# Kernel tuning notes

Hardware: AMD Instinct MI355X
Metric: run time of the kernel (lower is better)

Reference implementation:

```python
import jax, jax.numpy as jnp
import numpy as np

KERNEL_SIZE = (5, 5)  # kernel_size repeated over dim=2 -> K = 25
DEGREE = 1            # linear B-spline
IS_OPEN = (1, 1)      # open splines in both pseudo-coordinate dims


def spline_basis(pseudo):
    """Degree-1 B-spline basis, matching torch_spline_conv SplineBasis.
    pseudo: [E, D] in [0, 1]. Returns basis [E, S], weight_index [E, S],
    with S = (degree+1)^D."""
    E, D = pseudo.shape
    m = DEGREE
    S = (m + 1) ** D
    ks = jnp.asarray(KERNEL_SIZE, dtype=jnp.int32)
    open_ = jnp.asarray(IS_OPEN, dtype=jnp.int32)
    v = pseudo * (ks - m * open_).astype(pseudo.dtype)          # [E, D]
    fl = jnp.floor(v)
    frac = v - fl                                                # fractional part
    fl = fl.astype(jnp.int32)
    # k_mod[s, d] = (s // (m+1)^d) % (m+1)  (mixed-radix digit)
    s_ids = jnp.arange(S, dtype=jnp.int32)
    radix = (m + 1) ** jnp.arange(D, dtype=jnp.int32)
    k_mod = (s_ids[:, None] // radix[None, :]) % (m + 1)         # [S, D]
    # degree-1 basis: k_mod==0 -> 1-frac ; k_mod==1 -> frac
    b = jnp.where(k_mod[None] == 0, 1.0 - frac[:, None, :], frac[:, None, :])  # [E,S,D]
    basis = jnp.prod(b, axis=-1)                                 # [E, S]
    # weight index: mixed-radix over kernel dims with wrap-around mod ks
    offs = jnp.concatenate([jnp.ones((1,), jnp.int32), jnp.cumprod(ks)[:-1]])  # [D]
    wi = jnp.sum(((fl[:, None, :] + k_mod[None]) % ks) * offs, axis=-1)        # [E, S]
    return basis, wi


def setup_inputs() -> dict:
    key = jax.random.key(0)
    k1, k2, k3, k4 = jax.random.split(key, 4)
    B, N, Fin, Fout, K = 8, 4096, 64, 64, 25
    x = jax.random.normal(k1, (B, N, Fin), dtype=jnp.float32)
    coord = jax.random.uniform(k2, (B, N, 2), dtype=jnp.float32)
    mask = jnp.ones((B, N), dtype=jnp.float32)
    weight = jax.random.normal(k3, (K, Fin, Fout), dtype=jnp.float32) * (1.0 / np.sqrt(K * Fin))
    root = jax.random.normal(k4, (Fin, Fout), dtype=jnp.float32) * (1.0 / np.sqrt(K * Fin))
    bias = jnp.zeros((Fout,), dtype=jnp.float32)
    return {"x": x, "coord": coord, "mask": mask, "weight": weight, "root": root, "bias": bias}


def reference(x, coord, mask, weight, root, bias):
    B, N, F = x.shape
    E = B * N
    x2 = x.reshape(E, F)
    basis, wi = spline_basis(coord.reshape(E, coord.shape[-1]))   # [E,S], [E,S]
    nan = jnp.isnan(basis)
    basis = jnp.where(nan, 0.0, basis)
    wi = jnp.where(nan, 0, wi)
    # SplineWeighting: out[e,o] = sum_s basis[e,s] * (x[e] @ weight[wi[e,s]])
    proj = jnp.einsum('ef,kfo->keo', x2, weight)                  # [K, E, O]
    gath = proj[wi, jnp.arange(E)[:, None], :]                    # [E, S, O]
    out = jnp.einsum('es,eso->eo', basis, gath)                   # [E, O]
    out = out + x2 @ root                                         # root (self) transform
    out = out.reshape(B, N, -1) + bias
    out = out * mask[..., None]                                   # 2D mask path
    return out
```

## Files before the change

### kernel.cpp

```cpp
#include <hip/hip_runtime.h>
#include <hip/hip_bf16.h>


#define NACT  16
#define NPREP 32
#define CAP_B 128
#define NTILE 40

typedef __attribute__((ext_vector_type(8))) short bhalf8;
typedef __attribute__((ext_vector_type(4))) float f32x4;

__device__ __forceinline__ unsigned short f2bf(float f) {
    return __builtin_bit_cast(unsigned short, __float2bfloat16(f));
}

__global__ __launch_bounds__(1024) void k_prep(
    const float* __restrict__ coord, const float* __restrict__ weight,
    const float* __restrict__ root,
    int* __restrict__ cnt2, int* __restrict__ idx2,
    unsigned short* __restrict__ wtab, int E)
{
    __shared__ int lcnt[NACT];
    int tid = threadIdx.x, blk = blockIdx.x;
    if (tid < NACT) lcnt[tid] = 0;
    __syncthreads();
    int e = blk * 1024 + tid;
    int c = 0, lpos = 0;
    if (e < E) {
        float2 cc = *(const float2*)(coord + 2 * e);
        int i0 = (int)floorf(cc.x * 4.0f); if (i0 > 3) i0 = 3; if (i0 < 0) i0 = 0;
        int i1 = (int)floorf(cc.y * 4.0f); if (i1 > 3) i1 = 3; if (i1 < 0) i1 = 0;
        c = i0 + 4 * i1;
        lpos = atomicAdd(&lcnt[c], 1);
    }
    __syncthreads();
    if (e < E && lpos < CAP_B) idx2[(c * NPREP + blk) * CAP_B + lpos] = e;
    if (tid < NACT) {
        int v = lcnt[tid];
        cnt2[tid * NPREP + blk] = v < CAP_B ? v : CAP_B;
    }

    if (tid < 400) {
        int gi = blk * 400 + tid;
        int k = gi >> 9;
        int r = gi & 511;
        int o = r >> 3, g = r & 7;
        const float* wsrc = weight + k * 4096;
        bhalf8 u8;
        #pragma unroll
        for (int j = 0; j < 8; ++j) {
            int f = g * 8 + j;
            u8[j] = f2bf(wsrc[f * 64 + o] + root[f * 64 + o]);
        }
        *(bhalf8*)((char*)wtab + k * 8192 + o * 128 + ((g ^ (o & 7)) << 4)) = u8;
    }
}

__global__ __launch_bounds__(256) void k_main(
    const float* __restrict__ x, const float* __restrict__ coord,
    const float* __restrict__ mask, const float* __restrict__ bias,
    const int* __restrict__ cnt2, const int* __restrict__ idx2,
    const unsigned short* __restrict__ wtab, float* __restrict__ out)
{
    __shared__ __align__(16) unsigned short xs[64 * 64];
    __shared__ __align__(16) unsigned short wt[4 * 64 * 64];
    __shared__ float4 bsv[64];
    __shared__ float  msk[64];
    __shared__ int    eid[64];
    __shared__ float  bsh[64];
    __shared__ int    sprefix[NPREP + 1];

    int tid = threadIdx.x;
    int lane = tid & 63, wv = tid >> 6;

    int u = blockIdx.x / NTILE;
    int t = blockIdx.x - u * NTILE;
    int i0 = u & 3, i1 = u >> 2;

    int v = (lane < NPREP) ? cnt2[u * NPREP + lane] : 0;
    int s = v;
    #pragma unroll
    for (int d = 1; d < 32; d <<= 1) {
        int q = __shfl_up(s, d, 64);
        if (lane >= d) s += q;
    }
    int ncell = __shfl(s, NPREP - 1, 64);
    int npts = ncell - t * 64;
    if (npts <= 0) return;
    if (npts > 64) npts = 64;

    if (wv == 0) {
        if (lane < NPREP) sprefix[lane + 1] = s;
        if (lane == 0) sprefix[0] = 0;
        bsh[lane] = bias[lane];
        if (lane < npts) {
            int gpos = t * 64 + lane;
            int lo = 0, hi = NPREP;
            while (hi - lo > 1) {
                int mid = (lo + hi) >> 1;
                if (sprefix[mid] <= gpos) lo = mid; else hi = mid;
            }
            int e = idx2[(u * NPREP + lo) * CAP_B + (gpos - sprefix[lo])];
            eid[lane] = e;
            float2 cc = *(const float2*)(coord + 2 * e);
            float v0 = cc.x * 4.0f, v1 = cc.y * 4.0f;
            float f0 = v0 - floorf(v0), f1 = v1 - floorf(v1);
            float4 b4;
            b4.x = (1.f - f0) * (1.f - f1);
            b4.y = f0 * (1.f - f1);
            b4.z = (1.f - f0) * f1;
            b4.w = f0 * f1;
            bsv[lane] = b4;
            msk[lane] = mask[e];
        }
    }

    {
        int kw = (i0 + (wv & 1)) + 5 * (i1 + (wv >> 1));
        const char* wsrcp = (const char*)wtab + kw * 8192 + lane * 16;
        char* wdst = (char*)wt + wv * 8192 + lane * 16;
        #pragma unroll
        for (int j = 0; j < 8; ++j) {
            bhalf8 w8 = *(const bhalf8*)(wsrcp + j * 1024);
            *(bhalf8*)(wdst + j * 1024) = w8;
        }
    }
    __syncthreads();

    {
        int p = tid >> 2;
        if (p < npts) {
            int e = eid[p];
            const float4* xr = (const float4*)(x + (long)e * 64);
            int g0 = (tid & 3) * 2;
            #pragma unroll
            for (int gg = 0; gg < 2; ++gg) {
                int g = g0 + gg;
                float4 lo4 = xr[2 * g], hi4 = xr[2 * g + 1];
                bhalf8 u8;
                u8[0] = f2bf(lo4.x); u8[1] = f2bf(lo4.y); u8[2] = f2bf(lo4.z); u8[3] = f2bf(lo4.w);
                u8[4] = f2bf(hi4.x); u8[5] = f2bf(hi4.y); u8[6] = f2bf(hi4.z); u8[7] = f2bf(hi4.w);
                *(bhalf8*)((char*)xs + p * 128 + ((g ^ (p & 7)) << 4)) = u8;
            }
        }
    }
    __syncthreads();

    int wm = wv >> 1, wn = wv & 1;
    int lr = lane & 15, lg = lane >> 4;

    f32x4 zero4 = {0.f, 0.f, 0.f, 0.f};
    f32x4 acc[4][2][2];
    #pragma unroll
    for (int ss = 0; ss < 4; ++ss)
        #pragma unroll
        for (int m = 0; m < 2; ++m)
            #pragma unroll
            for (int n = 0; n < 2; ++n) acc[ss][m][n] = zero4;

    #pragma unroll
    for (int kk = 0; kk < 2; ++kk) {
        bhalf8 a[2];
        #pragma unroll
        for (int m = 0; m < 2; ++m) {
            int p = wm * 32 + m * 16 + lr;
            int g = kk * 4 + lg;
            a[m] = *(const bhalf8*)((const char*)xs + p * 128 + ((g ^ (p & 7)) << 4));
        }
        #pragma unroll
        for (int ss = 0; ss < 4; ++ss) {
            #pragma unroll
            for (int n = 0; n < 2; ++n) {
                int o = wn * 32 + n * 16 + lr;
                int g = kk * 4 + lg;
                bhalf8 b = *(const bhalf8*)((const char*)wt + ss * 8192 + o * 128 + ((g ^ (o & 7)) << 4));
                #pragma unroll
                for (int m = 0; m < 2; ++m)
                    acc[ss][m][n] = __builtin_amdgcn_mfma_f32_16x16x32_bf16(a[m], b, acc[ss][m][n], 0, 0, 0);
            }
        }
    }

    #pragma unroll
    for (int m = 0; m < 2; ++m) {
        #pragma unroll
        for (int n = 0; n < 2; ++n) {
            int col = wn * 32 + n * 16 + lr;
            int pb = wm * 32 + m * 16 + lg * 4;
            if (npts == 64) {
                #pragma unroll
                for (int r = 0; r < 4; ++r) {
                    int p = pb + r;
                    float4 b4 = bsv[p];
                    float vv = fmaf(b4.x, acc[0][m][n][r],
                               fmaf(b4.y, acc[1][m][n][r],
                               fmaf(b4.z, acc[2][m][n][r],
                                    b4.w * acc[3][m][n][r])));
                    vv = (vv + bsh[col]) * msk[p];
                    out[(long)eid[p] * 64 + col] = vv;
                }
            } else {
                #pragma unroll
                for (int r = 0; r < 4; ++r) {
                    int p = pb + r;
                    if (p < npts) {
                        float4 b4 = bsv[p];
                        float vv = fmaf(b4.x, acc[0][m][n][r],
                                   fmaf(b4.y, acc[1][m][n][r],
                                   fmaf(b4.z, acc[2][m][n][r],
                                        b4.w * acc[3][m][n][r])));
                        vv = (vv + bsh[col]) * msk[p];
                        out[(long)eid[p] * 64 + col] = vv;
                    }
                }
            }
        }
    }
}

extern "C" void kernel_launch(void* const* d_in, const int* in_sizes, int n_in,
                              void* d_out, int out_size, void* d_ws, size_t ws_size,
                              hipStream_t stream) {
    const float* x      = (const float*)d_in[0];
    const float* coord  = (const float*)d_in[1];
    const float* mask   = (const float*)d_in[2];
    const float* weight = (const float*)d_in[3];
    const float* root   = (const float*)d_in[4];
    const float* bias   = (const float*)d_in[5];
    float* out = (float*)d_out;

    const int E = in_sizes[2];

    char* ws = (char*)d_ws;
    int*            cnt2 = (int*)ws;
    int*            idx2 = (int*)(ws + 4096);
    unsigned short* wtab = (unsigned short*)(ws + 4096 + (size_t)NACT * NPREP * CAP_B * 4);

    k_prep<<<NPREP, 1024, 0, stream>>>(coord, weight, root, cnt2, idx2, wtab, E);
    k_main<<<NACT * NTILE, 256, 0, stream>>>(x, coord, mask, bias, cnt2, idx2, wtab, out);
}
```

Measured before the change: 17.26 us.

## Map main blocks directly to per-prep-block cell buckets, dropping scan and search

Each k_main block now handles one (cell, prep-block, half) bucket and reads its point count and indices directly. This removes the wave-level prefix scan over bucket counts and the per-lane binary search through an LDS prefix array. The grid grows from 640 to 1024 blocks. Many of the second-half blocks hold only a few points, so tiles are less full and the four shared weight tiles are loaded from L2 more times overall.

After: 21.01 us. 1.22x slower.

```diff
diff --git a/kernel.cpp b/kernel.cpp
--- a/kernel.cpp
+++ b/kernel.cpp
@@ -5,7 +5,6 @@
 #define NACT  16
 #define NPREP 32
 #define CAP_B 128
-#define NTILE 40
 
 typedef __attribute__((ext_vector_type(8))) short bhalf8;
 typedef __attribute__((ext_vector_type(4))) float f32x4;
@@ -68,39 +67,27 @@
     __shared__ float  msk[64];
     __shared__ int    eid[64];
     __shared__ float  bsh[64];
-    __shared__ int    sprefix[NPREP + 1];
 
     int tid = threadIdx.x;
     int lane = tid & 63, wv = tid >> 6;
 
-    int u = blockIdx.x / NTILE;
-    int t = blockIdx.x - u * NTILE;
+    int bid = blockIdx.x;
+    int t   = bid & 1;
+    int blk = (bid >> 1) & (NPREP - 1);
+    int u   = bid >> 6;
     int i0 = u & 3, i1 = u >> 2;
 
-    int v = (lane < NPREP) ? cnt2[u * NPREP + lane] : 0;
-    int s = v;
-    #pragma unroll
-    for (int d = 1; d < 32; d <<= 1) {
-        int q = __shfl_up(s, d, 64);
-        if (lane >= d) s += q;
-    }
-    int ncell = __shfl(s, NPREP - 1, 64);
-    int npts = ncell - t * 64;
+    int n = cnt2[u * NPREP + blk];
+    int npts = n - t * 64;
     if (npts <= 0) return;
     if (npts > 64) npts = 64;
 
+    int base = (u * NPREP + blk) * CAP_B + t * 64;
+
     if (wv == 0) {
-        if (lane < NPREP) sprefix[lane + 1] = s;
-        if (lane == 0) sprefix[0] = 0;
         bsh[lane] = bias[lane];
         if (lane < npts) {
-            int gpos = t * 64 + lane;
-            int lo = 0, hi = NPREP;
-            while (hi - lo > 1) {
-                int mid = (lo + hi) >> 1;
-                if (sprefix[mid] <= gpos) lo = mid; else hi = mid;
-            }
-            int e = idx2[(u * NPREP + lo) * CAP_B + (gpos - sprefix[lo])];
+            int e = idx2[base + lane];
             eid[lane] = e;
             float2 cc = *(const float2*)(coord + 2 * e);
             float v0 = cc.x * 4.0f, v1 = cc.y * 4.0f;
@@ -237,5 +224,5 @@
     unsigned short* wtab = (unsigned short*)(ws + 4096 + (size_t)NACT * NPREP * CAP_B * 4);
 
     k_prep<<<NPREP, 1024, 0, stream>>>(coord, weight, root, cnt2, idx2, wtab, E);
-    k_main<<<NACT * NTILE, 256, 0, stream>>>(x, coord, mask, bias, cnt2, idx2, wtab, out);
-}
+    k_main<<<NACT * NPREP * 2, 256, 0, stream>>>(x, coord, mask, bias, cnt2, idx2, wtab, out);
+}
```
